# Performance work log

Measured on AMD Instinct MI355X. Metric: run time of the kernel, lower is better.

## Reference

```python
import jax, jax.numpy as jnp
import numpy as np

H = 16      # num heads
DH = 64     # head dim
D = H * DH  # hidden = 1024

def setup_inputs() -> dict:
    key = jax.random.key(0)
    ks = jax.random.split(key, 8)
    B, S = 4, 2048
    scale = 1.0 / np.sqrt(D)
    return {
        "hidden_states": jax.random.normal(ks[0], (B, S, D), dtype=jnp.float32),
        "attention_mask": jnp.zeros((B, S, S), dtype=jnp.float32),
        "Wq": jax.random.normal(ks[1], (D, D), dtype=jnp.float32) * scale,
        "bq": jnp.zeros((D,), dtype=jnp.float32),
        "Wk": jax.random.normal(ks[2], (D, D), dtype=jnp.float32) * scale,
        "bk": jnp.zeros((D,), dtype=jnp.float32),
        "Wv": jax.random.normal(ks[3], (D, D), dtype=jnp.float32) * scale,
        "bv": jnp.zeros((D,), dtype=jnp.float32),
    }

def _split_heads(x):
    B, S, _ = x.shape
    return x.reshape(B, S, H, DH).transpose(0, 2, 1, 3)  # [B,H,S,dh]

def reference(hidden_states, attention_mask, Wq, bq, Wk, bk, Wv, bv):
    q = _split_heads(hidden_states @ Wq + bq)
    k = _split_heads(hidden_states @ Wk + bk)
    v = _split_heads(hidden_states @ Wv + bv)
    scores = jnp.einsum("bhqd,bhkd->bhqk", q, k) / jnp.sqrt(jnp.float32(DH))
    scores = scores + attention_mask[:, None, :, :]
    probs = jax.nn.softmax(scores, axis=-1)  # dropout p=0 (eval) -> identity
    ctx = jnp.einsum("bhqk,bhkd->bhqd", probs, v)
    B, _, S, _ = ctx.shape
    return ctx.transpose(0, 2, 1, 3).reshape(B, S, H * DH)
```

## Files before the change

kernel.cpp:

```cpp
#include <hip/hip_runtime.h>

typedef __bf16 bf16;
typedef __bf16 bf16x8 __attribute__((ext_vector_type(8)));
typedef __bf16 bf16x4 __attribute__((ext_vector_type(4)));
typedef float floatx4 __attribute__((ext_vector_type(4)));
typedef unsigned int uint4t __attribute__((ext_vector_type(4)));

typedef __attribute__((address_space(1))) void gvoid;
typedef __attribute__((address_space(3))) void lvoid;
#define ASYNC_COPY16(gp, lp) \
  __builtin_amdgcn_global_load_lds((gvoid*)(gp), (lvoid*)(lp), 16, 0, 0)

#define NB 4
#define SQ 2048
#define DMODEL 1024
#define NH 16
#define HD 64
#define MTOK (NB * SQ)
#define LOG2E 1.44269504088896f

#define XB_OFF 0ull
#define WT_OFF (16ull * 1024 * 1024)
#define Q_OFF  (22ull * 1024 * 1024)
#define K_OFF  (38ull * 1024 * 1024)
#define V_OFF  (54ull * 1024 * 1024)
#define FLG_OFF (70ull * 1024 * 1024)

__global__ __launch_bounds__(256) void prep(
    const float* __restrict__ x, bf16* __restrict__ xb,
    const float* __restrict__ w0, const float* __restrict__ w1,
    const float* __restrict__ w2, bf16* __restrict__ wt,
    const float* __restrict__ mask, int* __restrict__ flags) {
  __shared__ float tlds[32][33];
  int blk = blockIdx.x;
  int t = threadIdx.x;
  if (blk < 1024) {
    size_t base = (size_t)blk * 2048 + t;
    const float4* xin = (const float4*)x;
    bf16x4* xo = (bf16x4*)xb;
#pragma unroll
    for (int j = 0; j < 8; j++) {
      float4 v = xin[base + j * 256];
      bf16x4 o;
      o[0] = (bf16)v.x; o[1] = (bf16)v.y; o[2] = (bf16)v.z; o[3] = (bf16)v.w;
      xo[base + j * 256] = o;
    }
  } else if (blk < 4096) {
    int tidx = blk - 1024;
    int z = tidx >> 10;
    int rem = tidx & 1023;
    int kb = ((rem >> 5) & 31) * 32, nb = (rem & 31) * 32;
    const float* w = (z == 0) ? w0 : (z == 1) ? w1 : w2;
    bf16* out = wt + (size_t)z * DMODEL * DMODEL;
    int tx = t & 31, ty = t >> 5;
#pragma unroll
    for (int i = 0; i < 4; i++)
      tlds[ty + 8 * i][tx] = w[(size_t)(kb + ty + 8 * i) * DMODEL + nb + tx];
    __syncthreads();
#pragma unroll
    for (int i = 0; i < 4; i++)
      out[(size_t)(nb + ty + 8 * i) * DMODEL + kb + tx] = (bf16)tlds[tx][ty + 8 * i];
  } else {
    int midx = blk - 4096;
    int kt = midx & 31, qt = (midx >> 5) & 15, b = midx >> 9;
    const float* mb = mask + ((size_t)b * SQ + qt * 128) * SQ + kt * 64;
    int row = t >> 1, half = t & 1;
    const float4* p = (const float4*)(mb + (size_t)row * SQ + half * 32);
    bool nz = false;
#pragma unroll
    for (int i = 0; i < 8; i++) {
      float4 vv = p[i];
      nz |= (vv.x != 0.f) | (vv.y != 0.f) | (vv.z != 0.f) | (vv.w != 0.f);
    }
    int* acc = (int*)tlds;
    if (t == 0) acc[0] = 0;
    __syncthreads();
    unsigned long long m = __ballot(nz);
    if ((t & 63) == 0 && m) atomicOr(acc, 1);
    __syncthreads();
    if (t == 0) flags[(b * 16 + qt) * 32 + kt] = acc[0];
  }
}

#define BK 64
__global__ __launch_bounds__(256) void qkv(
    const bf16* __restrict__ xb,
    const bf16* __restrict__ wt,
    const float* __restrict__ biasq, const float* __restrict__ biask,
    const float* __restrict__ biasv,
    bf16* __restrict__ q, bf16* __restrict__ k, bf16* __restrict__ v) {
  __shared__ bf16 smem[2 * 128 * BK];
  bf16* As = smem;
  bf16* Bs = smem + 128 * BK;

  int id = blockIdx.x;
  int local = id >> 3;
  int mt = ((id & 7) << 3) | (local & 7);
  int nt = local >> 3;
  int t = threadIdx.x;

  int mat = nt >> 3;
  int nbase = (nt & 7) * 128;
  const bf16* wmat = wt + (size_t)mat * DMODEL * DMODEL;
  const float* bias = (mat == 0) ? biasq : (mat == 1) ? biask : biasv;
  bf16* outp = (mat == 0) ? q : (mat == 1) ? k : v;

  int lane = t & 63, wid = t >> 6;
  int quad = lane >> 4, l16 = lane & 15;
  int wm = (wid & 1) * 64, wn = (wid >> 1) * 64;
  int xq = quad ^ (l16 & 7);

  floatx4 acc[4][4] = {};

  for (int kb = 0; kb < DMODEL; kb += BK) {
    __syncthreads();
#pragma unroll
    for (int p = 0; p < 4; p++) {
      int i2 = p * 256 + t;
      int row = i2 >> 3;
      int gch = (i2 ^ row) & 7;
      ASYNC_COPY16(xb + (size_t)(mt * 128 + row) * DMODEL + kb + gch * 8,
                   As + i2 * 8);
      ASYNC_COPY16(wmat + (size_t)(nbase + row) * DMODEL + kb + gch * 8,
                   Bs + i2 * 8);
    }
    __syncthreads();

#pragma unroll
    for (int kc = 0; kc < BK; kc += 32) {
      int xc = (kc >> 3) ^ xq;
      bf16x8 af[4], bfr[4];
#pragma unroll
      for (int mi = 0; mi < 4; mi++)
        af[mi] = *(const bf16x8*)(As + (wm + mi * 16 + l16) * BK + xc * 8);
#pragma unroll
      for (int ni = 0; ni < 4; ni++)
        bfr[ni] = *(const bf16x8*)(Bs + (wn + ni * 16 + l16) * BK + xc * 8);
      if (mat < 2) {
#pragma unroll
        for (int mi = 0; mi < 4; mi++)
#pragma unroll
          for (int ni = 0; ni < 4; ni++)
            acc[mi][ni] = __builtin_amdgcn_mfma_f32_16x16x32_bf16(
                bfr[ni], af[mi], acc[mi][ni], 0, 0, 0);
      } else {
#pragma unroll
        for (int mi = 0; mi < 4; mi++)
#pragma unroll
          for (int ni = 0; ni < 4; ni++)
            acc[mi][ni] = __builtin_amdgcn_mfma_f32_16x16x32_bf16(
                af[mi], bfr[ni], acc[mi][ni], 0, 0, 0);
      }
    }
  }

  int mg0 = mt * 128 + wm;
  if (mat < 2) {
    float qscale = (mat == 0) ? 0.125f * LOG2E : 1.0f;
    __syncthreads();
#pragma unroll
    for (int ni = 0; ni < 4; ni++) {
      int n0 = nbase + wn + ni * 16 + quad * 4;
      float4 bv4 = *(const float4*)(bias + n0);
      int nc = wn + ni * 16 + quad * 4;
      int unit = nc >> 3, h8 = (nc >> 2) & 1;
#pragma unroll
      for (int mi = 0; mi < 4; mi++) {
        int sr = wm + mi * 16 + l16;
        bf16x4 pk;
        pk[0] = (bf16)((acc[mi][ni][0] + bv4.x) * qscale);
        pk[1] = (bf16)((acc[mi][ni][1] + bv4.y) * qscale);
        pk[2] = (bf16)((acc[mi][ni][2] + bv4.z) * qscale);
        pk[3] = (bf16)((acc[mi][ni][3] + bv4.w) * qscale);
        int su = unit ^ (sr & 15);
        *(bf16x4*)(smem + sr * 128 + su * 8 + h8 * 4) = pk;
      }
    }
    __syncthreads();
    int sr = t >> 1, half = t & 1;
    int bb = mt >> 4;
    int s = ((mt & 15) << 7) + sr;
    int h = (nbase >> 6) + half;
    bf16* gout = outp + (((size_t)(bb * NH + h) * SQ + s) << 6);
#pragma unroll
    for (int i = 0; i < 8; i++) {
      int su = (half * 8 + i) ^ (sr & 15);
      bf16x8 ch = *(const bf16x8*)(smem + sr * 128 + su * 8);
      *(bf16x8*)(gout + i * 8) = ch;
    }
  } else {
#pragma unroll
    for (int ni = 0; ni < 4; ni++) {
      int n = nbase + wn + ni * 16 + l16;
      int h = n >> 6, d = n & 63;
      float bv_ = bias[n];
#pragma unroll
      for (int mi = 0; mi < 4; mi++) {
        int m0 = mg0 + mi * 16 + quad * 4;
        int b = m0 >> 11, s = m0 & 2047;
        bf16x4 pk;
#pragma unroll
        for (int r = 0; r < 4; r++) pk[r] = (bf16)(acc[mi][ni][r] + bv_);
        *(bf16x4*)(outp + (((size_t)(b * NH + h) * HD + d) << 11) + s) = pk;
      }
    }
  }
}

__global__ __launch_bounds__(256, 4) void attn(
    const bf16* __restrict__ Q,
    const bf16* __restrict__ K,
    const bf16* __restrict__ Vt,
    const float* __restrict__ mask,
    const int* __restrict__ flags,
    float* __restrict__ out) {
  __shared__ bf16 Ks[64 * 64];
  __shared__ bf16 Vs[64 * 64];

  int bh = blockIdx.x;
  int qt = blockIdx.y;
  int b = bh >> 4, h = bh & 15;
  int t = threadIdx.x, lane = t & 63, wid = t >> 6;
  int quad = lane >> 4, l16 = lane & 15;
  int q0 = qt * 128 + wid * 32;

  const bf16* Qp = Q + ((size_t)bh * SQ + q0) * HD;
  const bf16* Kp = K + (size_t)bh * SQ * HD;
  const bf16* Vp = Vt + (size_t)bh * HD * SQ;
  const float* mp = mask + ((size_t)b * SQ + q0) * SQ;
  const int* flg = flags + (b * 16 + qt) * 32;

  bf16x8 qa[2][2];
#pragma unroll
  for (int m = 0; m < 2; m++) {
    const bf16* qr = Qp + (size_t)(m * 16 + l16) * HD;
    qa[m][0] = *(const bf16x8*)(qr + quad * 8);
    qa[m][1] = *(const bf16x8*)(qr + 32 + quad * 8);
  }

  floatx4 o[2][4] = {};
  float li[2] = {0.f, 0.f};
  int xq = quad ^ (l16 & 7);

  for (int kb = 0, kti = 0; kb < SQ; kb += 64, kti++) {
    __syncthreads();
#pragma unroll
    for (int p = 0; p < 2; p++) {
      int idx = p * 256 + t;
      int row = idx >> 3;
      int gch = (idx ^ row) & 7;
      ASYNC_COPY16(Kp + (size_t)(kb + row) * HD + gch * 8, Ks + idx * 8);
      ASYNC_COPY16(Vp + (size_t)row * SQ + kb + gch * 8, Vs + idx * 8);
    }
    __syncthreads();
    int flag = flg[kti];

    float xs[2][4][4];
    __builtin_amdgcn_s_setprio(1);
#pragma unroll
    for (int kt = 0; kt < 4; kt++) {
      const bf16* kr = Ks + (kt * 16 + l16) * 64;
      bf16x8 k0 = *(const bf16x8*)(kr + xq * 8);
      bf16x8 k1 = *(const bf16x8*)(kr + (xq ^ 4) * 8);
      floatx4 z0 = {}, z1 = {};
      z0 = __builtin_amdgcn_mfma_f32_16x16x32_bf16(k0, qa[0][0], z0, 0, 0, 0);
      z0 = __builtin_amdgcn_mfma_f32_16x16x32_bf16(k1, qa[0][1], z0, 0, 0, 0);
      z1 = __builtin_amdgcn_mfma_f32_16x16x32_bf16(k0, qa[1][0], z1, 0, 0, 0);
      z1 = __builtin_amdgcn_mfma_f32_16x16x32_bf16(k1, qa[1][1], z1, 0, 0, 0);
#pragma unroll
      for (int r = 0; r < 4; r++) { xs[0][kt][r] = z0[r]; xs[1][kt][r] = z1[r]; }
    }
    __builtin_amdgcn_s_setprio(0);
    if (flag) {
#pragma unroll
      for (int m = 0; m < 2; m++)
#pragma unroll
        for (int kt = 0; kt < 4; kt++)
#pragma unroll
          for (int r = 0; r < 4; r++)
            xs[m][kt][r] = __builtin_fmaf(
                mp[(size_t)(m * 16 + l16) * SQ + kb + kt * 16 + quad * 4 + r],
                LOG2E, xs[m][kt][r]);
    }

    bf16x8 pb[2][2];
#pragma unroll
    for (int m = 0; m < 2; m++) {
      float sum = 0.f;
      unsigned int u[4][2];
#pragma unroll
      for (int kt = 0; kt < 4; kt++) {
        float e0 = __builtin_amdgcn_exp2f(xs[m][kt][0]);
        float e1 = __builtin_amdgcn_exp2f(xs[m][kt][1]);
        float e2 = __builtin_amdgcn_exp2f(xs[m][kt][2]);
        float e3 = __builtin_amdgcn_exp2f(xs[m][kt][3]);
        sum += (e0 + e1) + (e2 + e3);
        asm("v_cvt_pk_bf16_f32 %0, %1, %2" : "=v"(u[kt][0]) : "v"(e0), "v"(e1));
        asm("v_cvt_pk_bf16_f32 %0, %1, %2" : "=v"(u[kt][1]) : "v"(e2), "v"(e3));
      }
      li[m] += sum;
#pragma unroll
      for (int f = 0; f < 2; f++) {
        unsigned int a0 = u[2 * f][0], b0 = u[2 * f + 1][0];
        unsigned int a1 = u[2 * f][1], b1 = u[2 * f + 1][1];
        asm("v_permlane32_swap_b32 %0, %1" : "+v"(a0), "+v"(b0));
        asm("v_permlane32_swap_b32 %0, %1" : "+v"(a1), "+v"(b1));
        asm("v_permlane16_swap_b32 %0, %1" : "+v"(a0), "+v"(b0));
        asm("v_permlane16_swap_b32 %0, %1" : "+v"(a1), "+v"(b1));
        uint4t w;
        w[0] = a0; w[1] = a1; w[2] = b0; w[3] = b1;
        pb[m][f] = __builtin_bit_cast(bf16x8, w);
      }
    }

    __builtin_amdgcn_s_setprio(1);
#pragma unroll
    for (int dt = 0; dt < 4; dt++) {
      const bf16* vr = Vs + (dt * 16 + l16) * 64;
      bf16x8 v0 = *(const bf16x8*)(vr + xq * 8);
      bf16x8 v1 = *(const bf16x8*)(vr + (xq ^ 4) * 8);
      o[0][dt] = __builtin_amdgcn_mfma_f32_16x16x32_bf16(v0, pb[0][0], o[0][dt], 0, 0, 0);
      o[0][dt] = __builtin_amdgcn_mfma_f32_16x16x32_bf16(v1, pb[0][1], o[0][dt], 0, 0, 0);
      o[1][dt] = __builtin_amdgcn_mfma_f32_16x16x32_bf16(v0, pb[1][0], o[1][dt], 0, 0, 0);
      o[1][dt] = __builtin_amdgcn_mfma_f32_16x16x32_bf16(v1, pb[1][1], o[1][dt], 0, 0, 0);
    }
    __builtin_amdgcn_s_setprio(0);
  }
#pragma unroll
  for (int m = 0; m < 2; m++) {
    li[m] += __shfl_xor(li[m], 16, 64);
    li[m] += __shfl_xor(li[m], 32, 64);
  }
#pragma unroll
  for (int m = 0; m < 2; m++) {
    float inv = 1.0f / li[m];
    float* op = out + ((size_t)b * SQ + q0 + m * 16 + l16) * DMODEL + h * HD;
#pragma unroll
    for (int dt = 0; dt < 4; dt++)
#pragma unroll
      for (int r = 0; r < 4; r++)
        op[dt * 16 + quad * 4 + r] = o[m][dt][r] * inv;
  }
}

extern "C" void kernel_launch(void* const* d_in, const int* in_sizes, int n_in,
                              void* d_out, int out_size, void* d_ws, size_t ws_size,
                              hipStream_t stream) {
  (void)in_sizes; (void)n_in; (void)out_size; (void)ws_size;
  const float* hs   = (const float*)d_in[0];
  const float* mask = (const float*)d_in[1];
  const float* Wq   = (const float*)d_in[2];
  const float* bq   = (const float*)d_in[3];
  const float* Wk   = (const float*)d_in[4];
  const float* bk   = (const float*)d_in[5];
  const float* Wv   = (const float*)d_in[6];
  const float* bv   = (const float*)d_in[7];
  float* out = (float*)d_out;
  char* ws = (char*)d_ws;
  bf16* xb = (bf16*)(ws + XB_OFF);
  bf16* wt = (bf16*)(ws + WT_OFF);
  bf16* q  = (bf16*)(ws + Q_OFF);
  bf16* k  = (bf16*)(ws + K_OFF);
  bf16* v  = (bf16*)(ws + V_OFF);
  int* flg = (int*)(ws + FLG_OFF);

  prep<<<1024 + 3072 + 2048, 256, 0, stream>>>(hs, xb, Wq, Wk, Wv, wt, mask, flg);
  qkv<<<1536, 256, 0, stream>>>(xb, wt, bq, bk, bv, q, k, v);
  attn<<<dim3(64, 16), 256, 0, stream>>>(q, k, v, mask, flg, out);
}
```

Before: 289.9 us.

## Switch attention inner loop from 16x16x32 to 32x32x16 MFMA tiles

Rewrites the attention kernel's QK^T and PV products to use 32x32x16 bf16 MFMA instructions instead of 16x16x32, which changes the register fragment layout for Q, P and the output accumulator. P packing now needs only permlane32 swaps, and the softmax row sum needs a single cross-lane shuffle. The epilogue writes output as float4 vectors instead of scalar stores. Each 32x32 MFMA does more work per instruction and shares LDS fragment reads, but the larger accumulators raise register pressure, and the LDS access pattern under the swizzle changes.

```diff
diff --git a/kernel.cpp b/kernel.cpp
--- a/kernel.cpp
+++ b/kernel.cpp
@@ -4,6 +4,7 @@
 typedef __bf16 bf16x8 __attribute__((ext_vector_type(8)));
 typedef __bf16 bf16x4 __attribute__((ext_vector_type(4)));
 typedef float floatx4 __attribute__((ext_vector_type(4)));
+typedef float floatx16 __attribute__((ext_vector_type(16)));
 typedef unsigned int uint4t __attribute__((ext_vector_type(4)));
 
 typedef __attribute__((address_space(1))) void gvoid;
@@ -221,7 +222,7 @@
   int qt = blockIdx.y;
   int b = bh >> 4, h = bh & 15;
   int t = threadIdx.x, lane = t & 63, wid = t >> 6;
-  int quad = lane >> 4, l16 = lane & 15;
+  int l32 = lane & 31, hi = lane >> 5;
   int q0 = qt * 128 + wid * 32;
 
   const bf16* Qp = Q + ((size_t)bh * SQ + q0) * HD;
@@ -230,17 +231,13 @@
   const float* mp = mask + ((size_t)b * SQ + q0) * SQ;
   const int* flg = flags + (b * 16 + qt) * 32;
 
-  bf16x8 qa[2][2];
-#pragma unroll
-  for (int m = 0; m < 2; m++) {
-    const bf16* qr = Qp + (size_t)(m * 16 + l16) * HD;
-    qa[m][0] = *(const bf16x8*)(qr + quad * 8);
-    qa[m][1] = *(const bf16x8*)(qr + 32 + quad * 8);
-  }
-
-  floatx4 o[2][4] = {};
-  float li[2] = {0.f, 0.f};
-  int xq = quad ^ (l16 & 7);
+  bf16x8 qa[4];
+#pragma unroll
+  for (int dp = 0; dp < 4; dp++)
+    qa[dp] = *(const bf16x8*)(Qp + (size_t)l32 * HD + dp * 16 + hi * 8);
+
+  floatx16 o2[2] = {};
+  float li = 0.f;
 
   for (int kb = 0, kti = 0; kb < SQ; kb += 64, kti++) {
     __syncthreads();
@@ -255,92 +252,82 @@
     __syncthreads();
     int flag = flg[kti];
 
-    float xs[2][4][4];
+    bf16x8 pf[2][2];
+#pragma unroll
+    for (int kt = 0; kt < 2; kt++) {
+      int row = kt * 32 + l32;
+      const bf16* kr = Ks + row * 64;
+      floatx16 z = {};
+      __builtin_amdgcn_s_setprio(1);
+#pragma unroll
+      for (int dp = 0; dp < 4; dp++) {
+        int ch = (dp * 2 + hi) ^ (row & 7);
+        bf16x8 kf = *(const bf16x8*)(kr + ch * 8);
+        z = __builtin_amdgcn_mfma_f32_32x32x16_bf16(kf, qa[dp], z, 0, 0, 0);
+      }
+      __builtin_amdgcn_s_setprio(0);
+      if (flag) {
+#pragma unroll
+        for (int r = 0; r < 16; r++) {
+          int kk = kb + kt * 32 + (r & 3) + 8 * (r >> 2) + 4 * hi;
+          z[r] = __builtin_fmaf(mp[(size_t)l32 * SQ + kk], LOG2E, z[r]);
+        }
+      }
+      float e[16];
+      float s = 0.f;
+#pragma unroll
+      for (int r = 0; r < 16; r++) {
+        e[r] = __builtin_amdgcn_exp2f(z[r]);
+        s += e[r];
+      }
+      li += s;
+#pragma unroll
+      for (int kp = 0; kp < 2; kp++) {
+        int bs = kp * 8;
+        unsigned int u0, u1, u2, u3;
+        asm("v_cvt_pk_bf16_f32 %0, %1, %2" : "=v"(u0) : "v"(e[bs + 0]), "v"(e[bs + 1]));
+        asm("v_cvt_pk_bf16_f32 %0, %1, %2" : "=v"(u1) : "v"(e[bs + 2]), "v"(e[bs + 3]));
+        asm("v_cvt_pk_bf16_f32 %0, %1, %2" : "=v"(u2) : "v"(e[bs + 4]), "v"(e[bs + 5]));
+        asm("v_cvt_pk_bf16_f32 %0, %1, %2" : "=v"(u3) : "v"(e[bs + 6]), "v"(e[bs + 7]));
+        asm("v_permlane32_swap_b32 %0, %1" : "+v"(u0), "+v"(u2));
+        asm("v_permlane32_swap_b32 %0, %1" : "+v"(u1), "+v"(u3));
+        uint4t w;
+        w[0] = u0; w[1] = u1; w[2] = u2; w[3] = u3;
+        pf[kt][kp] = __builtin_bit_cast(bf16x8, w);
+      }
+    }
+
     __builtin_amdgcn_s_setprio(1);
 #pragma unroll
-    for (int kt = 0; kt < 4; kt++) {
-      const bf16* kr = Ks + (kt * 16 + l16) * 64;
-      bf16x8 k0 = *(const bf16x8*)(kr + xq * 8);
-      bf16x8 k1 = *(const bf16x8*)(kr + (xq ^ 4) * 8);
-      floatx4 z0 = {}, z1 = {};
-      z0 = __builtin_amdgcn_mfma_f32_16x16x32_bf16(k0, qa[0][0], z0, 0, 0, 0);
-      z0 = __builtin_amdgcn_mfma_f32_16x16x32_bf16(k1, qa[0][1], z0, 0, 0, 0);
-      z1 = __builtin_amdgcn_mfma_f32_16x16x32_bf16(k0, qa[1][0], z1, 0, 0, 0);
-      z1 = __builtin_amdgcn_mfma_f32_16x16x32_bf16(k1, qa[1][1], z1, 0, 0, 0);
-#pragma unroll
-      for (int r = 0; r < 4; r++) { xs[0][kt][r] = z0[r]; xs[1][kt][r] = z1[r]; }
-    }
-    __builtin_amdgcn_s_setprio(0);
-    if (flag) {
-#pragma unroll
-      for (int m = 0; m < 2; m++)
-#pragma unroll
-        for (int kt = 0; kt < 4; kt++)
-#pragma unroll
-          for (int r = 0; r < 4; r++)
-            xs[m][kt][r] = __builtin_fmaf(
-                mp[(size_t)(m * 16 + l16) * SQ + kb + kt * 16 + quad * 4 + r],
-                LOG2E, xs[m][kt][r]);
-    }
-
-    bf16x8 pb[2][2];
-#pragma unroll
-    for (int m = 0; m < 2; m++) {
-      float sum = 0.f;
-      unsigned int u[4][2];
-#pragma unroll
-      for (int kt = 0; kt < 4; kt++) {
-        float e0 = __builtin_amdgcn_exp2f(xs[m][kt][0]);
-        float e1 = __builtin_amdgcn_exp2f(xs[m][kt][1]);
-        float e2 = __builtin_amdgcn_exp2f(xs[m][kt][2]);
-        float e3 = __builtin_amdgcn_exp2f(xs[m][kt][3]);
-        sum += (e0 + e1) + (e2 + e3);
-        asm("v_cvt_pk_bf16_f32 %0, %1, %2" : "=v"(u[kt][0]) : "v"(e0), "v"(e1));
-        asm("v_cvt_pk_bf16_f32 %0, %1, %2" : "=v"(u[kt][1]) : "v"(e2), "v"(e3));
-      }
-      li[m] += sum;
-#pragma unroll
-      for (int f = 0; f < 2; f++) {
-        unsigned int a0 = u[2 * f][0], b0 = u[2 * f + 1][0];
-        unsigned int a1 = u[2 * f][1], b1 = u[2 * f + 1][1];
-        asm("v_permlane32_swap_b32 %0, %1" : "+v"(a0), "+v"(b0));
-        asm("v_permlane32_swap_b32 %0, %1" : "+v"(a1), "+v"(b1));
-        asm("v_permlane16_swap_b32 %0, %1" : "+v"(a0), "+v"(b0));
-        asm("v_permlane16_swap_b32 %0, %1" : "+v"(a1), "+v"(b1));
-        uint4t w;
-        w[0] = a0; w[1] = a1; w[2] = b0; w[3] = b1;
-        pb[m][f] = __builtin_bit_cast(bf16x8, w);
-      }
-    }
-
-    __builtin_amdgcn_s_setprio(1);
-#pragma unroll
-    for (int dt = 0; dt < 4; dt++) {
-      const bf16* vr = Vs + (dt * 16 + l16) * 64;
-      bf16x8 v0 = *(const bf16x8*)(vr + xq * 8);
-      bf16x8 v1 = *(const bf16x8*)(vr + (xq ^ 4) * 8);
-      o[0][dt] = __builtin_amdgcn_mfma_f32_16x16x32_bf16(v0, pb[0][0], o[0][dt], 0, 0, 0);
-      o[0][dt] = __builtin_amdgcn_mfma_f32_16x16x32_bf16(v1, pb[0][1], o[0][dt], 0, 0, 0);
-      o[1][dt] = __builtin_amdgcn_mfma_f32_16x16x32_bf16(v0, pb[1][0], o[1][dt], 0, 0, 0);
-      o[1][dt] = __builtin_amdgcn_mfma_f32_16x16x32_bf16(v1, pb[1][1], o[1][dt], 0, 0, 0);
+    for (int dt = 0; dt < 2; dt++) {
+      int row = dt * 32 + l32;
+      const bf16* vr = Vs + row * 64;
+#pragma unroll
+      for (int kt = 0; kt < 2; kt++)
+#pragma unroll
+        for (int kp = 0; kp < 2; kp++) {
+          int ch = (kt * 4 + kp * 2 + hi) ^ (row & 7);
+          bf16x8 vf = *(const bf16x8*)(vr + ch * 8);
+          o2[dt] = __builtin_amdgcn_mfma_f32_32x32x16_bf16(vf, pf[kt][kp], o2[dt], 0, 0, 0);
+        }
     }
     __builtin_amdgcn_s_setprio(0);
   }
-#pragma unroll
-  for (int m = 0; m < 2; m++) {
-    li[m] += __shfl_xor(li[m], 16, 64);
-    li[m] += __shfl_xor(li[m], 32, 64);
-  }
-#pragma unroll
-  for (int m = 0; m < 2; m++) {
-    float inv = 1.0f / li[m];
-    float* op = out + ((size_t)b * SQ + q0 + m * 16 + l16) * DMODEL + h * HD;
-#pragma unroll
-    for (int dt = 0; dt < 4; dt++)
-#pragma unroll
-      for (int r = 0; r < 4; r++)
-        op[dt * 16 + quad * 4 + r] = o[m][dt][r] * inv;
-  }
+
+  li += __shfl_xor(li, 32, 64);
+  float inv = 1.0f / li;
+  float* op = out + ((size_t)b * SQ + q0 + l32) * DMODEL + h * HD;
+#pragma unroll
+  for (int dt = 0; dt < 2; dt++)
+#pragma unroll
+    for (int g = 0; g < 4; g++) {
+      float4 w;
+      w.x = o2[dt][g * 4 + 0] * inv;
+      w.y = o2[dt][g * 4 + 1] * inv;
+      w.z = o2[dt][g * 4 + 2] * inv;
+      w.w = o2[dt][g * 4 + 3] * inv;
+      *(float4*)(op + dt * 32 + g * 8 + hi * 4) = w;
+    }
 }
 
 extern "C" void kernel_launch(void* const* d_in, const int* in_sizes, int n_in,
```

Result: slower. 299.7 us (+3.4%).
